# Kernel optimization log

Hardware: AMD Instinct MI355X
Metric: run time of the kernel (lower is better)

Reference implementation:

```python
import jax, jax.numpy as jnp
import numpy as np

B, L = 2, 4096
EMBED_DIM, NUM_HEADS, WINDOW = 1024, 16, 256
NUM_EXPERTS, TOP_K, FF_HIDDEN = 8, 2, 4096
ENTROPY_W, MAX_USAGE = 0.1, 0.3


def setup_inputs() -> dict:
    key = jax.random.key(0)
    ks = jax.random.split(key, 10)
    s = 0.02
    C, F, E = EMBED_DIM, FF_HIDDEN, NUM_EXPERTS
    return {
        "x": jax.random.normal(ks[0], (B, L, C), jnp.float32),
        "g1": jnp.ones((C,), jnp.float32), "b1": jnp.zeros((C,), jnp.float32),
        "g2": jnp.ones((C,), jnp.float32), "b2": jnp.zeros((C,), jnp.float32),
        "g3": jnp.ones((C,), jnp.float32), "b3": jnp.zeros((C,), jnp.float32),
        "Wqkv": jax.random.normal(ks[1], (C, 3 * C), jnp.float32) * s, "bqkv": jnp.zeros((3 * C,), jnp.float32),
        "Wo": jax.random.normal(ks[2], (C, C), jnp.float32) * s, "bo": jnp.zeros((C,), jnp.float32),
        "conv_w": jax.random.normal(ks[3], (C, C, 3), jnp.float32) * s, "conv_b": jnp.zeros((C,), jnp.float32),
        "gate_W": jax.random.normal(ks[4], (C, E), jnp.float32) * s, "gate_b": jnp.zeros((E,), jnp.float32),
        "expert_W": jax.random.normal(ks[5], (E, C, C), jnp.float32) * s, "expert_b": jnp.zeros((E, C), jnp.float32),
        "ff_W1": jax.random.normal(ks[6], (C, F), jnp.float32) * s, "ff_b1": jnp.zeros((F,), jnp.float32),
        "ff_W2": jax.random.normal(ks[7], (F, C), jnp.float32) * s, "ff_b2": jnp.zeros((C,), jnp.float32),
    }


def _ln(x, g, b):
    mu = x.mean(-1, keepdims=True)
    var = ((x - mu) ** 2).mean(-1, keepdims=True)
    return (x - mu) * jax.lax.rsqrt(var + 1e-5) * g + b


def _local_attn(x, Wqkv, bqkv, Wo, bo):
    # Faithful port of the unfold-based overlapping-window attention
    Bsz, Ln, C = x.shape
    hd = C // NUM_HEADS
    pad = (-Ln) % WINDOW
    xp = jnp.pad(x, ((0, 0), (0, pad), (0, 0)))
    Lp = Ln + pad
    qkv = (xp @ Wqkv + bqkv).reshape(Bsz, Lp, 3, NUM_HEADS, hd).transpose(2, 0, 3, 1, 4)
    q, k, v = qkv[0], qkv[1], qkv[2]  # [B,H,Lp,hd]
    step = WINDOW // 2  # bidirectional=True -> overlapping windows
    nw = (Lp - WINDOW) // step + 1
    idx = (jnp.arange(nw) * step)[:, None] + jnp.arange(WINDOW)[None, :]  # [nw,w]

    def win(t):
        # torch unfold(dim=2,size=w,step) puts window on LAST axis -> [B,H,nw,hd,w]
        return jnp.swapaxes(t[:, :, idx, :], -1, -2)

    qw, kw, vw = win(q), win(k), win(v)
    # q @ k^T over the window axis (exactly what the torch code computes)
    attn = jax.nn.softmax(jnp.einsum('bhnds,bhnes->bhnde', qw, kw) * hd ** -0.5, axis=-1)
    o = jnp.einsum('bhnde,bhnes->bhnds', attn, vw)  # [B,H,nw,hd,w]
    o = o.reshape(Bsz, NUM_HEADS, nw * WINDOW, hd).transpose(0, 2, 1, 3).reshape(Bsz, nw * WINDOW, C)
    return (o @ Wo + bo)[:, :Ln]


def _dconv(x, w, b):
    # Conv1d(C,C,k=3,dilation=2,padding='same'); w is [O,I,K]
    y = jax.lax.conv_general_dilated(jnp.swapaxes(x, 1, 2), w, (1,), 'SAME',
                                     rhs_dilation=(2,), dimension_numbers=('NCH', 'OIH', 'NCH'))
    return jnp.swapaxes(y + b[None, :, None], 1, 2)


def _moe(x, gW, gb, eW, eb):
    Bsz, S, C = x.shape
    N = Bsz * S
    xf = x.reshape(N, C)
    probs = jax.nn.softmax(xf @ gW + gb, axis=-1)
    entropy = -jnp.sum(probs * jnp.log(probs + 1e-10), axis=-1).mean()
    topk_p, topk_i = jax.lax.top_k(probs, TOP_K)  # [N,K]
    # dense-equivalent top-k dispatch: out[n] = sum_k p_k * expert_{i_k}(x_n)
    eo = jnp.einsum('nc,ech->neh', xf, eW) + eb  # [N,E,C]
    combine = jnp.zeros((N, NUM_EXPERTS), xf.dtype).at[jnp.arange(N)[:, None], topk_i].add(topk_p)
    out = jnp.einsum('neh,ne->nh', eo, combine)
    counts = jnp.zeros((NUM_EXPERTS,), jnp.float32).at[topk_i.reshape(-1)].add(1.0)
    penalty = jnp.sum(jax.nn.relu(counts / N - MAX_USAGE))
    return out.reshape(Bsz, S, C), ENTROPY_W * entropy + penalty


def reference(x, g1, b1, g2, b2, g3, b3, Wqkv, bqkv, Wo, bo, conv_w, conv_b,
              gate_W, gate_b, expert_W, expert_b, ff_W1, ff_b1, ff_W2, ff_b2):
    x = x + _local_attn(_ln(x, g1, b1), Wqkv, bqkv, Wo, bo)
    x = x + _dconv(_ln(x, g2, b2), conv_w, conv_b)
    moe_out, aux = _moe(_ln(x, g3, b3), gate_W, gate_b, expert_W, expert_b)
    x = x + moe_out
    x = x + (jax.nn.gelu(x @ ff_W1 + ff_b1, approximate=False) @ ff_W2 + ff_b2)
    return x, aux
```

## Files before the change

### kernel.cpp

```cpp
#include <hip/hip_runtime.h>
#include <cmath>

typedef _Float16 f16;
typedef __attribute__((ext_vector_type(8))) _Float16 f16x8;
typedef __attribute__((ext_vector_type(4))) _Float16 f16x4;
typedef __attribute__((ext_vector_type(4))) float f32x4;

struct TileInfo { int m0, mcnt, e, pad; };

__device__ __forceinline__ void gload16(const void* g, void* l) {
  __builtin_amdgcn_global_load_lds((const __attribute__((address_space(1))) void*)g,
                                   (__attribute__((address_space(3))) void*)l, 16, 0, 0);
}

__device__ __forceinline__ float fast_gelu(float u) {
  const float c = u * (0.7978845608028654f + 0.0356774081f * u * u);
  const float t = fminf(2.0f * c, 80.0f);
  const float e = __expf(t);
  return u * (e * __builtin_amdgcn_rcpf(e + 1.0f));
}

template<int NPASS, int MODE, int EPI>
__global__ __launch_bounds__(256)
void gemm_kernel(const f16* __restrict__ Ah, const f16* __restrict__ Al, int lda,
                 const f16* __restrict__ Bh, const f16* __restrict__ Bl, int ldb,
                 const float* __restrict__ bias, const float* __restrict__ res,
                 float* __restrict__ outf, f16* __restrict__ outh, int ldo, int K,
                 const int* __restrict__ rowmap, const TileInfo* __restrict__ table,
                 const char* __restrict__ zbuf) {
  constexpr int BK = 64;
  constexpr int RB = BK * 2;
  constexpr int TB = 128 * RB;
  constexpr int ROUNDS = TB / 4096;
  constexpr int TPR = RB / 16;
  constexpr int RPR = 4096 / RB;
  constexpr int SWM = TPR - 1;
  constexpr int LA  = 0;
  constexpr int LAL = (NPASS == 3) ? TB : 0;
  constexpr int LB  = (NPASS == 3) ? 2 * TB : TB;
  constexpr int LBL = (NPASS == 3) ? 3 * TB : 0;

  __shared__ __align__(16) char lds[(NPASS == 3) ? 65536 : 32768];

  const int tid  = threadIdx.x;
  const int wave = tid >> 6;
  const int lane = tid & 63;

  int m0, mcnt, eidx = 0;
  if (MODE == 2) {
    TileInfo ti = table[blockIdx.x];
    if (ti.mcnt <= 0) return;
    m0 = ti.m0; mcnt = ti.mcnt; eidx = ti.e;
  } else { m0 = blockIdx.x * 128; mcnt = 128; }
  const int n0 = blockIdx.y * 128;

  const f16* Bh_ = Bh;
  const float* bias_ = bias;
  size_t adelta = 0, bdelta = 0;
  if (NPASS == 3) {
    adelta = (size_t)((const char*)Al - (const char*)Ah);
    bdelta = (size_t)((const char*)Bl - (const char*)Bh);
  }
  if (MODE == 2) { Bh_ += ((size_t)eidx << 20); bias_ += eidx * 1024; }

  const int sr    = tid / TPR;
  const int cbyte = (tid % TPR) * 16;

  const char* aSrc[ROUNDS];
  const char* bSrc[ROUNDS];
  int aRowC[ROUNDS]; int aCbs[ROUNDS];
  #pragma unroll
  for (int r = 0; r < ROUNDS; ++r) {
    const int mr  = sr + r * RPR;
    const int cbs = cbyte ^ ((mr & SWM) << 4);
    int gi = m0 + ((mr < mcnt) ? mr : (mcnt - 1));
    if (MODE == 1 || MODE == 2) gi = rowmap[gi];
    if (MODE == 3) { aRowC[r] = gi; aCbs[r] = cbs; aSrc[r] = nullptr; }
    else           { aSrc[r] = (const char*)Ah + (size_t)gi * lda * 2 + cbs; aRowC[r] = 0; aCbs[r] = 0; }
    const int nr   = sr + r * RPR;
    const int ncbs = cbyte ^ ((nr & SWM) << 4);
    bSrc[r] = (const char*)Bh_ + (size_t)(n0 + nr) * ldb * 2 + ncbs;
  }

  f32x4 acc[4][4] = {};
  const int wm  = (wave >> 1) * 64;
  const int wn  = (wave & 1) * 64;
  const int fr  = lane & 15;
  const int kgb = (lane >> 4) * 16;

  for (int k0 = 0; k0 < K; k0 += BK) {
    #pragma unroll
    for (int r = 0; r < ROUNDS; ++r) {
      const char* as;
      const char* asl = nullptr;
      if (MODE == 3) {
        const int tap = k0 >> 10;
        const int kc  = k0 & 1023;
        const int tok = aRowC[r] & 4095;
        const int st  = tok + (tap - 1) * 2;
        if (st >= 0 && st < 4096) {
          as  = (const char*)Ah + (size_t)(aRowC[r] + (tap - 1) * 2) * 2048 + kc * 2 + aCbs[r];
          asl = as + adelta;
        } else {
          as  = zbuf;
          asl = zbuf;
        }
      } else {
        as = aSrc[r] + (size_t)k0 * 2;
        if (NPASS == 3) asl = as + adelta;
      }
      gload16(as, lds + LA + r * 4096 + wave * 1024);
      if (NPASS == 3) gload16(asl, lds + LAL + r * 4096 + wave * 1024);
      const char* bs = bSrc[r] + (size_t)k0 * 2;
      gload16(bs, lds + LB + r * 4096 + wave * 1024);
      if (NPASS == 3) gload16(bs + bdelta, lds + LBL + r * 4096 + wave * 1024);
    }
    __syncthreads();
    #pragma unroll
    for (int kk = 0; kk < BK / 32; ++kk) {
      f16x8 ah[4], bh[4], al[4], bl[4];
      #pragma unroll
      for (int i = 0; i < 4; ++i) {
        const int ar = wm + i * 16 + fr;
        const int ao = ar * RB + ((kk * 64 + kgb) ^ ((ar & SWM) << 4));
        ah[i] = *(const f16x8*)(lds + LA + ao);
        if (NPASS == 3) al[i] = *(const f16x8*)(lds + LAL + ao);
        const int br = wn + i * 16 + fr;
        const int bo = br * RB + ((kk * 64 + kgb) ^ ((br & SWM) << 4));
        bh[i] = *(const f16x8*)(lds + LB + bo);
        if (NPASS == 3) bl[i] = *(const f16x8*)(lds + LBL + bo);
      }
      #pragma unroll
      for (int i = 0; i < 4; ++i) {
        #pragma unroll
        for (int j = 0; j < 4; ++j) {
          acc[i][j] = __builtin_amdgcn_mfma_f32_16x16x32_f16(ah[i], bh[j], acc[i][j], 0, 0, 0);
          if (NPASS == 3) {
            acc[i][j] = __builtin_amdgcn_mfma_f32_16x16x32_f16(ah[i], bl[j], acc[i][j], 0, 0, 0);
            acc[i][j] = __builtin_amdgcn_mfma_f32_16x16x32_f16(al[i], bh[j], acc[i][j], 0, 0, 0);
          }
        }
      }
    }
    __syncthreads();
  }

  #pragma unroll
  for (int i = 0; i < 4; ++i) {
    const int mb = wm + i * 16 + (lane >> 4) * 4;
    #pragma unroll
    for (int j = 0; j < 4; ++j) {
      const int nc = n0 + wn + j * 16 + fr;
      const float bv = bias_[nc];
      #pragma unroll
      for (int q = 0; q < 4; ++q) {
        const int ml = mb + q;
        if (MODE == 2 && ml >= mcnt) continue;
        const size_t orow = (size_t)(m0 + ml);
        float v = acc[i][j][q] + bv;
        if (EPI == 1) v += res[orow * ldo + nc];
        if (EPI == 3) v = fast_gelu(v);
        if (EPI <= 1) outf[orow * ldo + nc] = v;
        else          outh[orow * ldo + nc] = (f16)v;
      }
    }
  }
}

template<int WLO, int WGATE>
__global__ __launch_bounds__(256)
void ln_kernel(const float* __restrict__ x, const float* __restrict__ g, const float* __restrict__ b,
               f16* __restrict__ oh, f16* __restrict__ ol,
               const float* __restrict__ gW, const float* __restrict__ gb,
               float* __restrict__ logits) {
  const int row = blockIdx.x;
  const int t = threadIdx.x;
  const float4 v = ((const float4*)(x + (size_t)row * 1024))[t];
  float s  = v.x + v.y + v.z + v.w;
  float ss = v.x * v.x + v.y * v.y + v.z * v.z + v.w * v.w;
  #pragma unroll
  for (int off = 32; off; off >>= 1) { s += __shfl_down(s, off, 64); ss += __shfl_down(ss, off, 64); }
  __shared__ float red[8];
  if ((t & 63) == 0) { red[t >> 6] = s; red[(t >> 6) + 4] = ss; }
  __syncthreads();
  s  = red[0] + red[1] + red[2] + red[3];
  ss = red[4] + red[5] + red[6] + red[7];
  const float mu  = s * (1.0f / 1024.0f);
  const float var = ss * (1.0f / 1024.0f) - mu * mu;
  const float inv = 1.0f / sqrtf(var + 1e-5f);
  const float4 gv = ((const float4*)g)[t];
  const float4 bv = ((const float4*)b)[t];
  float y[4];
  y[0] = (v.x - mu) * inv * gv.x + bv.x;
  y[1] = (v.y - mu) * inv * gv.y + bv.y;
  y[2] = (v.z - mu) * inv * gv.z + bv.z;
  y[3] = (v.w - mu) * inv * gv.w + bv.w;
  f16x4 hv;
  #pragma unroll
  for (int u = 0; u < 4; ++u) hv[u] = (f16)y[u];
  *(f16x4*)(oh + (size_t)row * 1024 + t * 4) = hv;
  if (WLO) {
    f16x4 lv;
    #pragma unroll
    for (int u = 0; u < 4; ++u) lv[u] = (f16)(y[u] - (float)hv[u]);
    *(f16x4*)(ol + (size_t)row * 1024 + t * 4) = lv;
  }
  if (WGATE) {
    const float* gr = gW + (size_t)(t * 4) * 8;
    float lg[8];
    #pragma unroll
    for (int e = 0; e < 8; ++e)
      lg[e] = y[0] * gr[e] + y[1] * gr[8 + e] + y[2] * gr[16 + e] + y[3] * gr[24 + e];
    #pragma unroll
    for (int m = 1; m < 64; m <<= 1)
      #pragma unroll
      for (int e = 0; e < 8; ++e) lg[e] += __shfl_xor(lg[e], m, 64);
    __shared__ float gred[4][8];
    if ((t & 63) == 0) {
      #pragma unroll
      for (int e = 0; e < 8; ++e) gred[t >> 6][e] = lg[e];
    }
    __syncthreads();
    if (t < 8)
      logits[(size_t)row * 8 + t] = gred[0][t] + gred[1][t] + gred[2][t] + gred[3][t] + gb[t];
  }
}

__global__ __launch_bounds__(512, 4)
void attn_kernel(const float* __restrict__ qkv, f16* __restrict__ oh, f16* __restrict__ ol) {
  __shared__ __align__(16) char sm[81920];
  const int bid = blockIdx.x;
  const int b = bid >> 8, h = (bid >> 4) & 15, n = bid & 15;
  const int t = threadIdx.x;
  const size_t rowbase = (size_t)(b * 2176 + n * 128);
  const char* qg = (const char*)(qkv + rowbase * 3072 + h * 64);
  const char* kg = qg + 4096;
  const char* vg = qg + 8192;

  const int srow = t >> 4;
  const int scol = (t & 15) * 16;
  const int wuni = (t >> 6) * 1024;

  const int dt = t >> 4;
  const int et = t & 15;
  float pacc[2][4] = {};

  for (int r = 0; r < 2; ++r) {
    #pragma unroll
    for (int p = 0; p < 4; ++p) {
      const size_t off = (size_t)(r * 128 + p * 32 + srow) * 12288 + scol;
      gload16(qg + off, sm + p * 8192 + wuni);
      gload16(kg + off, sm + 32768 + p * 8192 + wuni);
    }
    __syncthreads();
    #pragma unroll 4
    for (int s = 0; s < 128; ++s) {
      const float2 q2 = *(const float2*)(sm + s * 256 + dt * 8);
      const f32x4 k4 = *(const f32x4*)(sm + 32768 + s * 256 + et * 16);
      #pragma unroll
      for (int z = 0; z < 4; ++z) {
        pacc[0][z] += q2.x * k4[z];
        pacc[1][z] += q2.y * k4[z];
      }
    }
    __syncthreads();
  }

  #pragma unroll
  for (int i = 0; i < 2; ++i) {
    #pragma unroll
    for (int z = 0; z < 4; ++z) pacc[i][z] *= 0.125f;
    float m = fmaxf(fmaxf(pacc[i][0], pacc[i][1]), fmaxf(pacc[i][2], pacc[i][3]));
    m = fmaxf(m, __shfl_xor(m, 1, 16));
    m = fmaxf(m, __shfl_xor(m, 2, 16));
    m = fmaxf(m, __shfl_xor(m, 4, 16));
    m = fmaxf(m, __shfl_xor(m, 8, 16));
    float den = 0.0f;
    #pragma unroll
    for (int z = 0; z < 4; ++z) { pacc[i][z] = expf(pacc[i][z] - m); den += pacc[i][z]; }
    den += __shfl_xor(den, 1, 16);
    den += __shfl_xor(den, 2, 16);
    den += __shfl_xor(den, 4, 16);
    den += __shfl_xor(den, 8, 16);
    const float dinv = 1.0f / den;
    f32x4 pv;
    #pragma unroll
    for (int z = 0; z < 4; ++z) pv[z] = pacc[i][z] * dinv;
    *(f32x4*)(sm + 65536 + (dt * 2 + i) * 256 + et * 16) = pv;
  }

  const int dt2 = t & 15;
  const int st  = t >> 4;
  const int ch  = h * 64 + (st & 15) * 4;
  const size_t rb2 = (size_t)(b * 4096 + n * 256);

  for (int c = 0; c < 2; ++c) {
    __syncthreads();
    #pragma unroll
    for (int p = 0; p < 4; ++p) {
      const size_t off = (size_t)(c * 128 + p * 32 + srow) * 12288 + scol;
      gload16(vg + off, sm + p * 8192 + wuni);
    }
    __syncthreads();
    float o[16];
    #pragma unroll
    for (int u = 0; u < 16; ++u) o[u] = 0.0f;
    #pragma unroll 2
    for (int e4 = 0; e4 < 16; ++e4) {
      f32x4 p4[4], v4[4];
      #pragma unroll
      for (int i = 0; i < 4; ++i)
        p4[i] = *(const f32x4*)(sm + 65536 + (dt2 * 4 + i) * 256 + e4 * 16);
      #pragma unroll
      for (int j = 0; j < 4; ++j)
        v4[j] = *(const f32x4*)(sm + (st * 4 + j) * 256 + e4 * 16);
      #pragma unroll
      for (int j = 0; j < 4; ++j)
        #pragma unroll
        for (int i = 0; i < 4; ++i) {
          o[j * 4 + i] += v4[j][0] * p4[i][0] + v4[j][1] * p4[i][1]
                        + v4[j][2] * p4[i][2] + v4[j][3] * p4[i][3];
        }
    }
    const int rq = c * 2 + (st >> 4);
    #pragma unroll
    for (int i = 0; i < 4; ++i) {
      const size_t row = rb2 + (size_t)(dt2 * 4 + i) * 4 + rq;
      f16x4 hv, lv;
      #pragma unroll
      for (int j = 0; j < 4; ++j) {
        const float val = o[j * 4 + i];
        hv[j] = (f16)val;
        lv[j] = (f16)(val - (float)hv[j]);
      }
      *(f16x4*)(oh + row * 1024 + ch) = hv;
      *(f16x4*)(ol + row * 1024 + ch) = lv;
    }
  }
}

template<int SPLIT>
__global__ __launch_bounds__(256)
void transpose_kernel(const float* __restrict__ in, int R, int Cc,
                      f16* __restrict__ oh, f16* __restrict__ ol) {
  __shared__ float tile[32][33];
  const size_t mat = (size_t)blockIdx.z * R * Cc;
  in += mat; oh += mat; if (SPLIT) ol += mat;
  const int tx = threadIdx.x & 31, ty = threadIdx.x >> 5;
  const int c = blockIdx.x * 32 + tx;
  #pragma unroll
  for (int j = 0; j < 32; j += 8) {
    const int r = blockIdx.y * 32 + ty + j;
    tile[ty + j][tx] = in[(size_t)r * Cc + c];
  }
  __syncthreads();
  const int rT = blockIdx.y * 32 + tx;
  #pragma unroll
  for (int j = 0; j < 32; j += 8) {
    const int cT = blockIdx.x * 32 + ty + j;
    const float v = tile[tx][ty + j];
    const f16 hv = (f16)v;
    oh[(size_t)cT * R + rT] = hv;
    if (SPLIT) ol[(size_t)cT * R + rT] = (f16)(v - (float)hv);
  }
}

__global__ __launch_bounds__(256)
void convw_kernel(const float* __restrict__ w, f16* __restrict__ oh, f16* __restrict__ ol) {
  const int id = blockIdx.x * 256 + threadIdx.x;
  const int o = id >> 10, i = id & 1023;
  const float* ws = w + (size_t)o * 3072 + i * 3;
  #pragma unroll
  for (int tap = 0; tap < 3; ++tap) {
    const float v = ws[tap];
    const f16 hv = (f16)v;
    const size_t oi = (size_t)o * 3072 + tap * 1024 + i;
    oh[oi] = hv;
    ol[oi] = (f16)(v - (float)hv);
  }
}

__global__ void qkvrows_kernel(int* __restrict__ rows) {
  const int r = blockIdx.x * 256 + threadIdx.x;
  if (r < 4352) rows[r] = (r >= 2176) ? (4096 + r - 2176) : r;
}

__global__ __launch_bounds__(256)
void gatefin_kernel(const float* __restrict__ logits, float* __restrict__ top2p,
                    int* __restrict__ top2i, float* __restrict__ ent,
                    int* __restrict__ counts) {
  __shared__ int hist[8];
  const int t = threadIdx.x;
  if (t < 8) hist[t] = 0;
  __syncthreads();
  const int token = blockIdx.x * 256 + t;
  float lg[8];
  const float4 l0 = ((const float4*)(logits + (size_t)token * 8))[0];
  const float4 l1 = ((const float4*)(logits + (size_t)token * 8))[1];
  lg[0] = l0.x; lg[1] = l0.y; lg[2] = l0.z; lg[3] = l0.w;
  lg[4] = l1.x; lg[5] = l1.y; lg[6] = l1.z; lg[7] = l1.w;
  int i0 = 0; float v0 = lg[0];
  #pragma unroll
  for (int e = 1; e < 8; ++e) if (lg[e] > v0) { v0 = lg[e]; i0 = e; }
  int i1 = 0; float v1 = -1e30f;
  #pragma unroll
  for (int e = 0; e < 8; ++e) if (e != i0 && lg[e] > v1) { v1 = lg[e]; i1 = e; }
  float den = 0.0f; float pr[8];
  #pragma unroll
  for (int e = 0; e < 8; ++e) { pr[e] = expf(lg[e] - v0); den += pr[e]; }
  const float dinv = 1.0f / den;
  float H = 0.0f, p0 = 0.0f, p1 = 0.0f;
  #pragma unroll
  for (int e = 0; e < 8; ++e) {
    const float p = pr[e] * dinv;
    H -= p * logf(p + 1e-10f);
    if (e == i0) p0 = p;
    if (e == i1) p1 = p;
  }
  ent[token] = H;
  top2p[token * 2] = p0; top2p[token * 2 + 1] = p1;
  top2i[token * 2] = i0; top2i[token * 2 + 1] = i1;
  atomicAdd(&hist[i0], 1);
  atomicAdd(&hist[i1], 1);
  __syncthreads();
  if (t < 8) atomicAdd(&counts[t], hist[t]);
}

__global__ __launch_bounds__(256)
void scan_kernel(const float* __restrict__ ent, const int* __restrict__ counts,
                 int* __restrict__ offs, TileInfo* __restrict__ table, float* __restrict__ auxout) {
  __shared__ float red[256];
  const int t = threadIdx.x;
  float s = 0.0f;
  for (int k = 0; k < 32; ++k) s += ent[t + (k << 8)];
  red[t] = s; __syncthreads();
  for (int hh = 128; hh > 0; hh >>= 1) { if (t < hh) red[t] += red[t + hh]; __syncthreads(); }
  if (t == 0) {
    const float entmean = red[0] * (1.0f / 8192.0f);
    float pen = 0.0f; int off = 0; int nt = 0;
    for (int e = 0; e < 8; ++e) {
      const int c = counts[e];
      offs[e] = off;
      for (int m = 0; m < c; m += 128) {
        table[nt].m0 = off + m;
        table[nt].mcnt = (c - m < 128) ? (c - m) : 128;
        table[nt].e = e; table[nt].pad = 0;
        ++nt;
      }
      off += c;
      const float fr = (float)c * (1.0f / 8192.0f) - 0.3f;
      pen += (fr > 0.0f) ? fr : 0.0f;
    }
    for (; nt < 160; ++nt) { table[nt].m0 = 0; table[nt].mcnt = 0; table[nt].e = 0; table[nt].pad = 0; }
    auxout[0] = 0.1f * entmean + pen;
  }
}

__global__ __launch_bounds__(256)
void scatter_kernel(const int* __restrict__ top2i, const int* __restrict__ offs,
                    int* __restrict__ fill, int* __restrict__ moe_rows,
                    int* __restrict__ row2slot) {
  __shared__ int hist[8];
  __shared__ int base[8];
  const int t = threadIdx.x;
  if (t < 8) hist[t] = 0;
  __syncthreads();
  const int id = blockIdx.x * 256 + t;
  const int e = top2i[id];
  const int myrank = atomicAdd(&hist[e], 1);
  __syncthreads();
  if (t < 8) base[t] = atomicAdd(&fill[t], hist[t]);
  __syncthreads();
  const int row = offs[e] + base[e] + myrank;
  moe_rows[row] = id >> 1;
  row2slot[id] = row;
}

__global__ __launch_bounds__(256)
void combine_kernel(const float* __restrict__ x2, const f16* __restrict__ eo,
                    const float* __restrict__ top2p, const int* __restrict__ row2slot,
                    float* __restrict__ x3, f16* __restrict__ x3h) {
  const int n = blockIdx.x;
  const int t = threadIdx.x;
  const int r0 = row2slot[n * 2], r1 = row2slot[n * 2 + 1];
  const float p0 = top2p[n * 2], p1 = top2p[n * 2 + 1];
  const float4 xv = ((const float4*)(x2 + (size_t)n * 1024))[t];
  const f16x4 e0 = ((const f16x4*)(eo + (size_t)r0 * 1024))[t];
  const f16x4 e1 = ((const f16x4*)(eo + (size_t)r1 * 1024))[t];
  float4 o;
  o.x = xv.x + p0 * (float)e0[0] + p1 * (float)e1[0];
  o.y = xv.y + p0 * (float)e0[1] + p1 * (float)e1[1];
  o.z = xv.z + p0 * (float)e0[2] + p1 * (float)e1[2];
  o.w = xv.w + p0 * (float)e0[3] + p1 * (float)e1[3];
  ((float4*)(x3 + (size_t)n * 1024))[t] = o;
  f16x4 hv; hv[0] = (f16)o.x; hv[1] = (f16)o.y; hv[2] = (f16)o.z; hv[3] = (f16)o.w;
  ((f16x4*)(x3h + (size_t)n * 1024))[t] = hv;
}

extern "C" void kernel_launch(void* const* d_in, const int* in_sizes, int n_in,
                              void* d_out, int out_size, void* d_ws, size_t ws_size,
                              hipStream_t stream) {
  (void)in_sizes; (void)n_in; (void)out_size; (void)ws_size;
  const float* x     = (const float*)d_in[0];
  const float* g1    = (const float*)d_in[1];
  const float* b1    = (const float*)d_in[2];
  const float* g2    = (const float*)d_in[3];
  const float* b2    = (const float*)d_in[4];
  const float* g3    = (const float*)d_in[5];
  const float* b3    = (const float*)d_in[6];
  const float* Wqkv  = (const float*)d_in[7];
  const float* bqkv  = (const float*)d_in[8];
  const float* Wo    = (const float*)d_in[9];
  const float* bo    = (const float*)d_in[10];
  const float* convw = (const float*)d_in[11];
  const float* convb = (const float*)d_in[12];
  const float* gateW = (const float*)d_in[13];
  const float* gateb = (const float*)d_in[14];
  const float* expW  = (const float*)d_in[15];
  const float* expb  = (const float*)d_in[16];
  const float* ffW1  = (const float*)d_in[17];
  const float* ffb1  = (const float*)d_in[18];
  const float* ffW2  = (const float*)d_in[19];
  const float* ffb2  = (const float*)d_in[20];
  float* out = (float*)d_out;

  char* W = (char*)d_ws;
  f16* wqkvT_h = (f16*)(W + 0);
  f16* wqkvT_l = (f16*)(W + 6291456);
  f16* woT_h   = (f16*)(W + 12582912);
  f16* woT_l   = (f16*)(W + 14680064);
  f16* wcvT_h  = (f16*)(W + 16777216);
  f16* wcvT_l  = (f16*)(W + 23068672);
  f16* wexpT   = (f16*)(W + 29360128);
  f16* wff1T   = (f16*)(W + 46137344);
  f16* wff2T   = (f16*)(W + 54525952);
  char* META   = W + 62914560;
  int* counts    = (int*)(META);
  int* fill      = (int*)(META + 32);
  int* offs      = (int*)(META + 64);
  TileInfo* table = (TileInfo*)(META + 128);
  char* zbuf     = META + 3072;
  int* qkv_rows  = (int*)(META + 4096);
  float* ent     = (float*)(META + 24576);
  float* top2p   = (float*)(META + 57344);
  int* top2i     = (int*)(META + 122880);
  int* moe_rows  = (int*)(META + 188416);
  int* row2slot  = (int*)(META + 253952);
  float* logits  = (float*)(META + 327680);
  char* SA = W + 63963136;
  char* SB = W + 97517568;
  char* SC = W + 164626432;
  char* SD = W + 198180864;
  char* SE = W + 231735296;

  f16* ln1h = (f16*)SA;            f16* ln1l = (f16*)(SA + 16777216);
  f16* ln2h = ln1h;                f16* ln2l = ln1l;
  f16* ln3h = ln1h;                f16* x3h  = (f16*)(SA + 16777216);
  float* qkvbuf = (float*)SB;
  float* x2buf  = (float*)SB;
  f16*   hbuf   = (f16*)SB;
  f16* attnh = (f16*)SC;           f16* attnl = (f16*)(SC + 16777216);
  float* x1 = (float*)SD;
  f16* eobuf = (f16*)SD;
  float* x3 = (float*)SE;

  hipMemsetAsync((void*)META, 0, 4096, stream);

  dim3 blk(256);
  transpose_kernel<1><<<dim3(96, 32, 1), blk, 0, stream>>>(Wqkv, 1024, 3072, wqkvT_h, wqkvT_l);
  transpose_kernel<1><<<dim3(32, 32, 1), blk, 0, stream>>>(Wo, 1024, 1024, woT_h, woT_l);
  convw_kernel<<<4096, blk, 0, stream>>>(convw, wcvT_h, wcvT_l);
  transpose_kernel<0><<<dim3(32, 32, 8), blk, 0, stream>>>(expW, 1024, 1024, wexpT, nullptr);
  transpose_kernel<0><<<dim3(128, 32, 1), blk, 0, stream>>>(ffW1, 1024, 4096, wff1T, nullptr);
  transpose_kernel<0><<<dim3(32, 128, 1), blk, 0, stream>>>(ffW2, 4096, 1024, wff2T, nullptr);
  qkvrows_kernel<<<17, blk, 0, stream>>>(qkv_rows);

  ln_kernel<1, 0><<<8192, blk, 0, stream>>>(x, g1, b1, ln1h, ln1l, nullptr, nullptr, nullptr);
  gemm_kernel<3, 1, 0><<<dim3(34, 24), blk, 0, stream>>>(ln1h, ln1l, 1024, wqkvT_h, wqkvT_l, 1024,
      bqkv, nullptr, qkvbuf, nullptr, 3072, 1024, qkv_rows, nullptr, nullptr);
  attn_kernel<<<512, dim3(512), 0, stream>>>(qkvbuf, attnh, attnl);
  gemm_kernel<3, 0, 1><<<dim3(64, 8), blk, 0, stream>>>(attnh, attnl, 1024, woT_h, woT_l, 1024,
      bo, x, x1, nullptr, 1024, 1024, nullptr, nullptr, nullptr);
  ln_kernel<1, 0><<<8192, blk, 0, stream>>>(x1, g2, b2, ln2h, ln2l, nullptr, nullptr, nullptr);
  gemm_kernel<3, 3, 1><<<dim3(64, 8), blk, 0, stream>>>(ln2h, ln2l, 1024, wcvT_h, wcvT_l, 3072,
      convb, x1, x2buf, nullptr, 1024, 3072, nullptr, nullptr, zbuf);
  ln_kernel<0, 1><<<8192, blk, 0, stream>>>(x2buf, g3, b3, ln3h, nullptr, gateW, gateb, logits);
  gatefin_kernel<<<32, blk, 0, stream>>>(logits, top2p, top2i, ent, counts);
  scan_kernel<<<1, blk, 0, stream>>>(ent, counts, offs, table, out + 8388608);
  scatter_kernel<<<64, blk, 0, stream>>>(top2i, offs, fill, moe_rows, row2slot);
  gemm_kernel<1, 2, 2><<<dim3(136, 8), blk, 0, stream>>>(ln3h, nullptr, 1024, wexpT, nullptr, 1024,
      expb, nullptr, nullptr, eobuf, 1024, 1024, moe_rows, table, nullptr);
  combine_kernel<<<8192, blk, 0, stream>>>(x2buf, eobuf, top2p, row2slot, x3, x3h);
  gemm_kernel<1, 0, 3><<<dim3(64, 32), blk, 0, stream>>>(x3h, nullptr, 1024, wff1T, nullptr, 1024,
      ffb1, nullptr, nullptr, hbuf, 4096, 1024, nullptr, nullptr, nullptr);
  gemm_kernel<1, 0, 1><<<dim3(64, 8), blk, 0, stream>>>(hbuf, nullptr, 4096, wff2T, nullptr, 4096,
      ffb2, x3, out, nullptr, 1024, 4096, nullptr, nullptr, nullptr);
}
```

Before: 804.2 us.

## Double-buffer LDS in single-pass GEMM with two-stage prefetch; use fast exp/log

For the single-pass (NPASS==1) GEMM path, LDS staging now uses two 32KB buffers. Tiles k+2 are issued with global_load_lds while MFMAs run on the current tile, synchronised by explicit vmcnt/lgkmcnt waits and raw barriers. This overlaps memory latency with compute, at the cost of doubling LDS for that path, which may reduce occupancy. The attention softmax and the router also switch to __expf/__logf intrinsics, trading a little accuracy for cheaper transcendentals.

```diff
diff --git a/kernel.cpp b/kernel.cpp
--- a/kernel.cpp
+++ b/kernel.cpp
@@ -29,18 +29,18 @@
                  const int* __restrict__ rowmap, const TileInfo* __restrict__ table,
                  const char* __restrict__ zbuf) {
   constexpr int BK = 64;
-  constexpr int RB = BK * 2;
-  constexpr int TB = 128 * RB;
-  constexpr int ROUNDS = TB / 4096;
-  constexpr int TPR = RB / 16;
-  constexpr int RPR = 4096 / RB;
-  constexpr int SWM = TPR - 1;
+  constexpr int RB = 128;
+  constexpr int TB = 16384;
+  constexpr int ROUNDS = 4;
+  constexpr int TPR = 8;
+  constexpr int RPR = 32;
+  constexpr int SWM = 7;
   constexpr int LA  = 0;
   constexpr int LAL = (NPASS == 3) ? TB : 0;
   constexpr int LB  = (NPASS == 3) ? 2 * TB : TB;
   constexpr int LBL = (NPASS == 3) ? 3 * TB : 0;
 
-  __shared__ __align__(16) char lds[(NPASS == 3) ? 65536 : 32768];
+  __shared__ __align__(16) char lds[65536];
 
   const int tid  = threadIdx.x;
   const int wave = tid >> 6;
@@ -88,61 +88,112 @@
   const int fr  = lane & 15;
   const int kgb = (lane >> 4) * 16;
 
-  for (int k0 = 0; k0 < K; k0 += BK) {
+  if constexpr (NPASS == 1) {
+    const int NT = K / BK;
     #pragma unroll
     for (int r = 0; r < ROUNDS; ++r) {
-      const char* as;
-      const char* asl = nullptr;
-      if (MODE == 3) {
-        const int tap = k0 >> 10;
-        const int kc  = k0 & 1023;
-        const int tok = aRowC[r] & 4095;
-        const int st  = tok + (tap - 1) * 2;
-        if (st >= 0 && st < 4096) {
-          as  = (const char*)Ah + (size_t)(aRowC[r] + (tap - 1) * 2) * 2048 + kc * 2 + aCbs[r];
+      gload16(aSrc[r], lds + r * 4096 + wave * 1024);
+      gload16(bSrc[r], lds + 16384 + r * 4096 + wave * 1024);
+    }
+    #pragma unroll
+    for (int r = 0; r < ROUNDS; ++r) {
+      gload16(aSrc[r] + (size_t)BK * 2, lds + 32768 + r * 4096 + wave * 1024);
+      gload16(bSrc[r] + (size_t)BK * 2, lds + 32768 + 16384 + r * 4096 + wave * 1024);
+    }
+    asm volatile("s_waitcnt vmcnt(8)" ::: "memory");
+    __builtin_amdgcn_s_barrier();
+
+    for (int kt = 0; kt < NT; ++kt) {
+      const int c = kt & 1;
+      const char* LAp = lds + c * 32768;
+      const char* LBp = LAp + 16384;
+      f16x8 ah[2][4], bh[2][4];
+      #pragma unroll
+      for (int kk = 0; kk < 2; ++kk) {
+        #pragma unroll
+        for (int i = 0; i < 4; ++i) {
+          const int ar = wm + i * 16 + fr;
+          ah[kk][i] = *(const f16x8*)(LAp + ar * RB + ((kk * 64 + kgb) ^ ((ar & SWM) << 4)));
+          const int br = wn + i * 16 + fr;
+          bh[kk][i] = *(const f16x8*)(LBp + br * RB + ((kk * 64 + kgb) ^ ((br & SWM) << 4)));
+        }
+      }
+      asm volatile("s_waitcnt lgkmcnt(0)" ::: "memory");
+      __builtin_amdgcn_s_barrier();
+      if (kt + 2 < NT) {
+        const size_t ko = (size_t)(kt + 2) * BK * 2;
+        #pragma unroll
+        for (int r = 0; r < ROUNDS; ++r) {
+          gload16(aSrc[r] + ko, lds + c * 32768 + r * 4096 + wave * 1024);
+          gload16(bSrc[r] + ko, lds + c * 32768 + 16384 + r * 4096 + wave * 1024);
+        }
+      }
+      #pragma unroll
+      for (int kk = 0; kk < 2; ++kk)
+        #pragma unroll
+        for (int i = 0; i < 4; ++i)
+          #pragma unroll
+          for (int j = 0; j < 4; ++j)
+            acc[i][j] = __builtin_amdgcn_mfma_f32_16x16x32_f16(ah[kk][i], bh[kk][j], acc[i][j], 0, 0, 0);
+      if (kt + 2 < NT) asm volatile("s_waitcnt vmcnt(8)" ::: "memory");
+      else             asm volatile("s_waitcnt vmcnt(0)" ::: "memory");
+      __builtin_amdgcn_s_barrier();
+    }
+  } else {
+    for (int k0 = 0; k0 < K; k0 += BK) {
+      #pragma unroll
+      for (int r = 0; r < ROUNDS; ++r) {
+        const char* as;
+        const char* asl = nullptr;
+        if (MODE == 3) {
+          const int tap = k0 >> 10;
+          const int kc  = k0 & 1023;
+          const int tok = aRowC[r] & 4095;
+          const int st  = tok + (tap - 1) * 2;
+          if (st >= 0 && st < 4096) {
+            as  = (const char*)Ah + (size_t)(aRowC[r] + (tap - 1) * 2) * 2048 + kc * 2 + aCbs[r];
+            asl = as + adelta;
+          } else {
+            as  = zbuf;
+            asl = zbuf;
+          }
+        } else {
+          as  = aSrc[r] + (size_t)k0 * 2;
           asl = as + adelta;
-        } else {
-          as  = zbuf;
-          asl = zbuf;
         }
-      } else {
-        as = aSrc[r] + (size_t)k0 * 2;
-        if (NPASS == 3) asl = as + adelta;
-      }
-      gload16(as, lds + LA + r * 4096 + wave * 1024);
-      if (NPASS == 3) gload16(asl, lds + LAL + r * 4096 + wave * 1024);
-      const char* bs = bSrc[r] + (size_t)k0 * 2;
-      gload16(bs, lds + LB + r * 4096 + wave * 1024);
-      if (NPASS == 3) gload16(bs + bdelta, lds + LBL + r * 4096 + wave * 1024);
-    }
-    __syncthreads();
-    #pragma unroll
-    for (int kk = 0; kk < BK / 32; ++kk) {
-      f16x8 ah[4], bh[4], al[4], bl[4];
-      #pragma unroll
-      for (int i = 0; i < 4; ++i) {
-        const int ar = wm + i * 16 + fr;
-        const int ao = ar * RB + ((kk * 64 + kgb) ^ ((ar & SWM) << 4));
-        ah[i] = *(const f16x8*)(lds + LA + ao);
-        if (NPASS == 3) al[i] = *(const f16x8*)(lds + LAL + ao);
-        const int br = wn + i * 16 + fr;
-        const int bo = br * RB + ((kk * 64 + kgb) ^ ((br & SWM) << 4));
-        bh[i] = *(const f16x8*)(lds + LB + bo);
-        if (NPASS == 3) bl[i] = *(const f16x8*)(lds + LBL + bo);
-      }
-      #pragma unroll
-      for (int i = 0; i < 4; ++i) {
+        gload16(as, lds + LA + r * 4096 + wave * 1024);
+        gload16(asl, lds + LAL + r * 4096 + wave * 1024);
+        const char* bs = bSrc[r] + (size_t)k0 * 2;
+        gload16(bs, lds + LB + r * 4096 + wave * 1024);
+        gload16(bs + bdelta, lds + LBL + r * 4096 + wave * 1024);
+      }
+      __syncthreads();
+      #pragma unroll
+      for (int kk = 0; kk < 2; ++kk) {
+        f16x8 ah[4], bh[4], al[4], bl[4];
         #pragma unroll
-        for (int j = 0; j < 4; ++j) {
-          acc[i][j] = __builtin_amdgcn_mfma_f32_16x16x32_f16(ah[i], bh[j], acc[i][j], 0, 0, 0);
-          if (NPASS == 3) {
+        for (int i = 0; i < 4; ++i) {
+          const int ar = wm + i * 16 + fr;
+          const int ao = ar * RB + ((kk * 64 + kgb) ^ ((ar & SWM) << 4));
+          ah[i] = *(const f16x8*)(lds + LA + ao);
+          al[i] = *(const f16x8*)(lds + LAL + ao);
+          const int br = wn + i * 16 + fr;
+          const int bo = br * RB + ((kk * 64 + kgb) ^ ((br & SWM) << 4));
+          bh[i] = *(const f16x8*)(lds + LB + bo);
+          bl[i] = *(const f16x8*)(lds + LBL + bo);
+        }
+        #pragma unroll
+        for (int i = 0; i < 4; ++i) {
+          #pragma unroll
+          for (int j = 0; j < 4; ++j) {
+            acc[i][j] = __builtin_amdgcn_mfma_f32_16x16x32_f16(ah[i], bh[j], acc[i][j], 0, 0, 0);
             acc[i][j] = __builtin_amdgcn_mfma_f32_16x16x32_f16(ah[i], bl[j], acc[i][j], 0, 0, 0);
             acc[i][j] = __builtin_amdgcn_mfma_f32_16x16x32_f16(al[i], bh[j], acc[i][j], 0, 0, 0);
           }
         }
       }
-    }
-    __syncthreads();
+      __syncthreads();
+    }
   }
 
   #pragma unroll
@@ -277,7 +328,7 @@
     m = fmaxf(m, __shfl_xor(m, 8, 16));
     float den = 0.0f;
     #pragma unroll
-    for (int z = 0; z < 4; ++z) { pacc[i][z] = expf(pacc[i][z] - m); den += pacc[i][z]; }
+    for (int z = 0; z < 4; ++z) { pacc[i][z] = __expf(pacc[i][z] - m); den += pacc[i][z]; }
     den += __shfl_xor(den, 1, 16);
     den += __shfl_xor(den, 2, 16);
     den += __shfl_xor(den, 4, 16);
@@ -407,13 +458,13 @@
   for (int e = 0; e < 8; ++e) if (e != i0 && lg[e] > v1) { v1 = lg[e]; i1 = e; }
   float den = 0.0f; float pr[8];
   #pragma unroll
-  for (int e = 0; e < 8; ++e) { pr[e] = expf(lg[e] - v0); den += pr[e]; }
+  for (int e = 0; e < 8; ++e) { pr[e] = __expf(lg[e] - v0); den += pr[e]; }
   const float dinv = 1.0f / den;
   float H = 0.0f, p0 = 0.0f, p1 = 0.0f;
   #pragma unroll
   for (int e = 0; e < 8; ++e) {
     const float p = pr[e] * dinv;
-    H -= p * logf(p + 1e-10f);
+    H -= p * __logf(p + 1e-10f);
     if (e == i0) p0 = p;
     if (e == i1) p1 = p;
   }
```

Result: faster. 741.1 us (-7.9%).
